# Kernel optimization log

Hardware: AMD Instinct MI355X
Metric: run time of the kernel (lower is better)

## Reference

```python
import jax, jax.numpy as jnp
import numpy as np

B, L, P, W, T = 2048, 128, 8, 512, 128
DT = 0.01


def setup_inputs() -> dict:
    key = jax.random.key(0)
    ks = jax.random.split(key, 8)
    def lin(k, fan_in, fan_out):
        return jax.random.normal(k, (fan_out, fan_in), jnp.float32) / jnp.sqrt(jnp.float32(fan_in))
    return {
        "x0": jax.random.normal(ks[0], (B, L), jnp.float32),
        "ts": jnp.arange(T, dtype=jnp.float32) * DT,
        "args": jax.random.normal(ks[1], (B, P), jnp.float32),
        "W0": lin(ks[2], L + P, W), "b0": jnp.zeros((W,), jnp.float32),
        "W1": lin(ks[3], W, W),     "b1": jnp.zeros((W,), jnp.float32),
        "W2": lin(ks[4], W, L),     "b2": jnp.zeros((L,), jnp.float32),
    }


def _vf(y, args, W0, b0, W1, b1, W2, b2):
    # OdeMLP: concat state with params, then Linear/tanh MLP. y:[B,L], args:[B,P]
    h = jnp.concatenate([y, args], axis=-1)
    h = jnp.tanh(h @ W0.T + b0)
    h = jnp.tanh(h @ W1.T + b1)
    return h @ W2.T + b2


def reference(x0, ts, args, W0, b0, W1, b1, W2, b2):
    # Fixed-step Bosh3 (Bogacki-Shampine 3rd order) integration, saving at every ts.
    f = lambda y: _vf(y, args, W0, b0, W1, b1, W2, b2)
    dts = ts[1:] - ts[:-1]  # [T-1]

    def step(y, dt):
        k1 = f(y)
        k2 = f(y + 0.5 * dt * k1)
        k3 = f(y + 0.75 * dt * k2)
        y_next = y + dt * ((2.0 / 9.0) * k1 + (1.0 / 3.0) * k2 + (4.0 / 9.0) * k3)
        return y_next, y_next

    _, ys = jax.lax.scan(step, x0, dts)          # [T-1, B, L]
    ys = jnp.concatenate([x0[None], ys], axis=0)  # [T, B, L]
    return jnp.transpose(ys, (1, 0, 2))           # [B, T, L]
```

## Files before the change

kernel.cpp:

```cpp
#include <hip/hip_runtime.h>
#include <hip/hip_bf16.h>


#define B_ 2048
#define L_ 128
#define P_ 8
#define T_ 128
#define GT_ 64
#define NGRP (B_/GT_)
#define NBLK (NGRP*8)

typedef __attribute__((ext_vector_type(8))) short short8;
typedef __attribute__((ext_vector_type(4))) float f32x4;
typedef __attribute__((ext_vector_type(4))) unsigned int u32x4;

#define WTOT (800*512)
#define CNT_OFF (WTOT + 256)
#define EXB (CNT_OFF + 16384)
#define XSTR 160
#define GSTR (64*XSTR + 2*64*512)

#define VMW0 asm volatile("s_waitcnt vmcnt(0)" ::: "memory")
#define LKW0 asm volatile("s_waitcnt lgkmcnt(0)" ::: "memory")
#define SCHB __builtin_amdgcn_sched_barrier(0)

__device__ __forceinline__ unsigned short f2bf(float f){
  unsigned u = __builtin_bit_cast(unsigned, f);
  u += 0x7fffu + ((u >> 16) & 1u);
  return (unsigned short)(u >> 16);
}

__device__ __forceinline__ float tanh_fast(float x){
  float e = __expf(2.0f * x);
  return 1.0f - __fdividef(2.0f, e + 1.0f);
}

__device__ __forceinline__ short8 ld_dev(const unsigned short* p){
  u32x4 r;
  asm volatile("global_load_dwordx4 %0, %1, off sc0 sc1"
               : "=v"(r) : "v"(p) : "memory");
  return __builtin_bit_cast(short8, r);
}
__device__ __forceinline__ void st_dev16b(unsigned short* p, u32x4 v){
  asm volatile("global_store_dwordx4 %0, %1, off sc0 sc1"
               :: "v"(p), "v"(v) : "memory");
}
__device__ __forceinline__ void st_dev2(unsigned short* p, unsigned short v){
  unsigned vv = v;
  asm volatile("global_store_short %0, %1, off sc0 sc1"
               :: "v"(p), "v"(vv) : "memory");
}

__global__ void prep_weights(const float* __restrict__ W0,
                             const float* __restrict__ W1,
                             const float* __restrict__ W2,
                             const float* __restrict__ ts,
                             unsigned short* __restrict__ wp){
  int idx = blockIdx.x * blockDim.x + threadIdx.x;
  if (idx >= WTOT){
    int t = idx - WTOT;
    if (t < T_ - 1){
      float* dts = (float*)(wp + WTOT);
      dts[t] = ts[t+1] - ts[t];
    } else if (t >= T_ && t < T_ + 8192){
      ((unsigned*)(wp + CNT_OFF))[t - T_] = 0u;
    }
    return;
  }
  int e = idx & 511, f = idx >> 9;
  int j = e & 7, lane = e >> 3;
  int m = f / 100, r = f % 100;
  const float* src; int nt, kt, Korig;
  if (r < 20)      { src = W0; Korig = 136; nt = 4*m + r/5;        kt = r%5; }
  else if (r < 84) { int q = r-20; src = W1; Korig = 512; nt = 4*m + (q>>4); kt = q&15; }
  else             { src = W2; Korig = 512; nt = m;                kt = r-84; }
  int row = nt*16 + (lane & 15);
  int k   = kt*32 + ((lane >> 4) << 3) + j;
  float v = (k < Korig) ? src[row*Korig + k] : 0.0f;
  wp[idx] = f2bf(v);
}

__global__ __launch_bounds__(256, 1)
void ode_main(const float* __restrict__ x0,
              const float* __restrict__ args,
              const float* __restrict__ b0, const float* __restrict__ b1,
              const float* __restrict__ b2,
              unsigned short* wp,
              float* __restrict__ out){
  __shared__ __align__(16) unsigned short wlds[100*512];
  __shared__ __align__(16) unsigned short hstg[4][16][64];
  __shared__ float dtl[T_];

  const int tid  = threadIdx.x;
  const int lane = tid & 63;
  const int wv   = tid >> 6;
  const int lo   = lane & 15;
  const int hi   = lane >> 4;
  const int bid  = blockIdx.x;
  const int m    = (bid >> 3) & 7;
  const int g    = (bid & 7)*4 + (bid >> 6);
  const int r0   = g * GT_;

  unsigned* cnt = (unsigned*)(wp + CNT_OFF) + (g*4 + wv)*64;
  unsigned short* gx  = wp + EXB + (size_t)g * GSTR;
  unsigned short* h1b = gx  + 64*XSTR;
  unsigned short* h2b = h1b + 64*512;

  {
    const u32x4* s = (const u32x4*)(wp + (size_t)m * 51200);
    u32x4* d = (u32x4*)wlds;
    for (int i = tid; i < 6400; i += 256) d[i] = s[i];
  }
  if (tid < T_-1) dtl[tid] = ((const float*)(wp + WTOT))[tid];

  float b0v[4], b1v[4];
  #pragma unroll
  for (int n = 0; n < 4; ++n){
    b0v[n] = b0[(4*m + n)*16 + lo];
    b1v[n] = b1[(4*m + n)*16 + lo];
  }
  const int c3 = m*16 + lo;
  float b2v = b2[c3];

  float yr[4], yn[4];
  #pragma unroll
  for (int j = 0; j < 4; ++j){
    int row = wv*16 + 4*hi + j;
    float v = x0[(r0 + row)*L_ + c3];
    yr[j] = v;
    __builtin_nontemporal_store(v, &out[((r0 + row)*T_ + 0)*L_ + c3]);
    st_dev2(gx + row*XSTR + c3, f2bf(v));
  }
  if (m == 0){
    #pragma unroll
    for (int e = 0; e < 8; ++e){
      int idx = lane*8 + e;
      int row = wv*16 + (idx >> 5), cc = 128 + (idx & 31);
      unsigned short vv = (cc < 136) ? f2bf(args[(r0 + row)*P_ + (cc - 128)])
                                     : (unsigned short)0;
      st_dev2(gx + row*XSTR + cc, vv);
    }
  }
  __syncthreads();

  unsigned tgt = 8;
  auto sigpoll = [&]{
    if (lane == 0)
      __hip_atomic_fetch_add(cnt, 1u, __ATOMIC_RELAXED, __HIP_MEMORY_SCOPE_AGENT);
    unsigned v;
    do {
      v = 0;
      if (lane == 0)
        v = __hip_atomic_load(cnt, __ATOMIC_RELAXED, __HIP_MEMORY_SCOPE_AGENT);
      v = __shfl(v, 0);
      if (v < tgt) __builtin_amdgcn_s_sleep(1);
    } while (v < tgt);
    tgt += 8;
  };

  VMW0;
  sigpoll();

  const int arow = wv*16 + lo;
  const int aoff = hi << 3;
  const int r16 = lane >> 2, ch4 = lane & 3;
  const int xr16 = (lane & 31) >> 1, xch = lane & 1;

  auto publish_h = [&](unsigned short* hb){
    LKW0;
    u32x4 v0 = *(const u32x4*)&hstg[wv][r16][ch4*16];
    u32x4 v1 = *(const u32x4*)&hstg[wv][r16][ch4*16 + 8];
    unsigned short* dst = hb + (wv*16 + r16)*512 + m*64 + ch4*16;
    st_dev16b(dst, v0);
    st_dev16b(dst + 8, v1);
    VMW0;
  };

  auto phase1 = [&]{
    short8 xa[5];
    #pragma unroll
    for (int kt = 0; kt < 5; ++kt)
      xa[kt] = ld_dev(gx + arow*XSTR + kt*32 + aoff);
    VMW0; SCHB;
    f32x4 acc[4];
    #pragma unroll
    for (int n = 0; n < 4; ++n) acc[n] = f32x4{0,0,0,0};
    #pragma unroll
    for (int kt = 0; kt < 5; ++kt)
      #pragma unroll
      for (int n = 0; n < 4; ++n){
        short8 wf = *(const short8*)(wlds + (n*5 + kt)*512 + lane*8);
        acc[n] = __builtin_amdgcn_mfma_f32_16x16x32_bf16(xa[kt], wf, acc[n], 0, 0, 0);
      }
    #pragma unroll
    for (int n = 0; n < 4; ++n)
      #pragma unroll
      for (int j = 0; j < 4; ++j)
        hstg[wv][4*hi + j][n*16 + lo] = f2bf(tanh_fast(acc[n][j] + b0v[n]));
    publish_h(h1b);
    sigpoll();
  };

  auto phase2 = [&]{
    short8 ha[16];
    #pragma unroll
    for (int kt = 0; kt < 16; ++kt)
      ha[kt] = ld_dev(h1b + arow*512 + kt*32 + aoff);
    VMW0; SCHB;
    f32x4 acc[4];
    #pragma unroll
    for (int n = 0; n < 4; ++n) acc[n] = f32x4{0,0,0,0};
    #pragma unroll
    for (int kt = 0; kt < 16; ++kt)
      #pragma unroll
      for (int n = 0; n < 4; ++n){
        short8 wf = *(const short8*)(wlds + (20 + n*16 + kt)*512 + lane*8);
        acc[n] = __builtin_amdgcn_mfma_f32_16x16x32_bf16(ha[kt], wf, acc[n], 0, 0, 0);
      }
    #pragma unroll
    for (int n = 0; n < 4; ++n)
      #pragma unroll
      for (int j = 0; j < 4; ++j)
        hstg[wv][4*hi + j][n*16 + lo] = f2bf(tanh_fast(acc[n][j] + b1v[n]));
    publish_h(h2b);
    sigpoll();
  };

  for (int t = 1; t < T_; ++t){
    float dt = dtl[t-1];
    #pragma unroll 1
    for (int s = 0; s < 3; ++s){
      phase1();
      phase2();
      short8 h2a[16];
      #pragma unroll
      for (int kt = 0; kt < 16; ++kt)
        h2a[kt] = ld_dev(h2b + arow*512 + kt*32 + aoff);
      VMW0; SCHB;
      f32x4 a3 = f32x4{0,0,0,0};
      #pragma unroll
      for (int kt = 0; kt < 16; ++kt){
        short8 wf = *(const short8*)(wlds + (84 + kt)*512 + lane*8);
        a3 = __builtin_amdgcn_mfma_f32_16x16x32_bf16(h2a[kt], wf, a3, 0, 0, 0);
      }
      #pragma unroll
      for (int j = 0; j < 4; ++j){
        float k = a3[j] + b2v;
        float xs;
        if (s == 0){ yn[j] = yr[j] + dt*(2.0f/9.0f)*k; xs = yr[j] + 0.5f*dt*k; }
        else if (s == 1){ yn[j] += dt*(1.0f/3.0f)*k;   xs = yr[j] + 0.75f*dt*k; }
        else { yn[j] += dt*(4.0f/9.0f)*k; yr[j] = yn[j]; xs = yr[j]; }
        hstg[wv][4*hi + j][lo] = f2bf(xs);
      }
      LKW0;
      if (lane < 32){
        u32x4 v = *(const u32x4*)&hstg[wv][xr16][xch*8];
        st_dev16b(gx + (wv*16 + xr16)*XSTR + m*16 + xch*8, v);
      }
      VMW0;
      if (lane == 0)
        __hip_atomic_fetch_add(cnt, 1u, __ATOMIC_RELAXED, __HIP_MEMORY_SCOPE_AGENT);
      if (s == 2){
        #pragma unroll
        for (int j = 0; j < 4; ++j){
          int row = wv*16 + 4*hi + j;
          __builtin_nontemporal_store(yr[j], &out[((r0 + row)*T_ + t)*L_ + c3]);
        }
      }
      {
        unsigned v;
        do {
          v = 0;
          if (lane == 0)
            v = __hip_atomic_load(cnt, __ATOMIC_RELAXED, __HIP_MEMORY_SCOPE_AGENT);
          v = __shfl(v, 0);
          if (v < tgt) __builtin_amdgcn_s_sleep(1);
        } while (v < tgt);
        tgt += 8;
      }
    }
  }
}

extern "C" void kernel_launch(void* const* d_in, const int* in_sizes, int n_in,
                              void* d_out, int out_size, void* d_ws, size_t ws_size,
                              hipStream_t stream) {
  const float* x0   = (const float*)d_in[0];
  const float* ts   = (const float*)d_in[1];
  const float* args = (const float*)d_in[2];
  const float* W0   = (const float*)d_in[3];
  const float* b0   = (const float*)d_in[4];
  const float* W1   = (const float*)d_in[5];
  const float* b1   = (const float*)d_in[6];
  const float* W2   = (const float*)d_in[7];
  const float* b2   = (const float*)d_in[8];
  unsigned short* wp = (unsigned short*)d_ws;
  float* out = (float*)d_out;

  prep_weights<<<(WTOT + T_ + 8192 + 255)/256, 256, 0, stream>>>(W0, W1, W2, ts, wp);
  ode_main<<<NBLK, 256, 0, stream>>>(x0, args, b0, b1, b2, wp, out);
}
```

Before: 4.643 ms.

## Detect same-XCC groups at runtime and use L2-scoped coherent exchange loads/stores

Blocks are remapped so that m = bid>>5 and g = bid&31, which is meant to place all 8 blocks of a batch group on the same XCC. At startup each group checks this: every block reads its XCC id, the m==0 block writes a tag, and the others compare against it. If all 8 blocks agree, the exchange traffic uses sc0-only loads and stores, keeping it in the shared L2 instead of going through system-coherent sc1 accesses. Otherwise the kernel falls back to the old path. This relies on the dispatcher placing blocks round-robin across XCCs, and it adds a handshake at startup.

```diff
diff --git a/kernel.cpp b/kernel.cpp
--- a/kernel.cpp
+++ b/kernel.cpp
@@ -1,5 +1,6 @@
 #include <hip/hip_runtime.h>
 #include <hip/hip_bf16.h>
+#include <type_traits>
 
 
 #define B_ 2048
@@ -8,7 +9,7 @@
 #define T_ 128
 #define GT_ 64
 #define NGRP (B_/GT_)
-#define NBLK (NGRP*8)
+#define NBLK 256
 
 typedef __attribute__((ext_vector_type(8))) short short8;
 typedef __attribute__((ext_vector_type(4))) float f32x4;
@@ -16,9 +17,10 @@
 
 #define WTOT (800*512)
 #define CNT_OFF (WTOT + 256)
-#define EXB (CNT_OFF + 16384)
+#define EXB (CNT_OFF + 16768)
 #define XSTR 160
 #define GSTR (64*XSTR + 2*64*512)
+#define NZERO 8320
 
 #define VMW0 asm volatile("s_waitcnt vmcnt(0)" ::: "memory")
 #define LKW0 asm volatile("s_waitcnt lgkmcnt(0)" ::: "memory")
@@ -35,20 +37,23 @@
   return 1.0f - __fdividef(2.0f, e + 1.0f);
 }
 
-__device__ __forceinline__ short8 ld_dev(const unsigned short* p){
+template<bool COH> __device__ __forceinline__ short8 ld_ex(const unsigned short* p){
   u32x4 r;
-  asm volatile("global_load_dwordx4 %0, %1, off sc0 sc1"
-               : "=v"(r) : "v"(p) : "memory");
+  if constexpr (COH)
+    asm volatile("global_load_dwordx4 %0, %1, off sc0" : "=v"(r) : "v"(p) : "memory");
+  else
+    asm volatile("global_load_dwordx4 %0, %1, off sc0 sc1" : "=v"(r) : "v"(p) : "memory");
   return __builtin_bit_cast(short8, r);
 }
-__device__ __forceinline__ void st_dev16b(unsigned short* p, u32x4 v){
-  asm volatile("global_store_dwordx4 %0, %1, off sc0 sc1"
-               :: "v"(p), "v"(v) : "memory");
-}
-__device__ __forceinline__ void st_dev2(unsigned short* p, unsigned short v){
+template<bool COH> __device__ __forceinline__ void st_ex16(unsigned short* p, u32x4 v){
+  if constexpr (COH)
+    asm volatile("global_store_dwordx4 %0, %1, off sc0" :: "v"(p), "v"(v) : "memory");
+  else
+    asm volatile("global_store_dwordx4 %0, %1, off sc0 sc1" :: "v"(p), "v"(v) : "memory");
+}
+__device__ __forceinline__ void st2_l3(unsigned short* p, unsigned short v){
   unsigned vv = v;
-  asm volatile("global_store_short %0, %1, off sc0 sc1"
-               :: "v"(p), "v"(vv) : "memory");
+  asm volatile("global_store_short %0, %1, off sc0 sc1" :: "v"(p), "v"(vv) : "memory");
 }
 
 __global__ void prep_weights(const float* __restrict__ W0,
@@ -62,7 +67,7 @@
     if (t < T_ - 1){
       float* dts = (float*)(wp + WTOT);
       dts[t] = ts[t+1] - ts[t];
-    } else if (t >= T_ && t < T_ + 8192){
+    } else if (t >= T_ && t < T_ + NZERO){
       ((unsigned*)(wp + CNT_OFF))[t - T_] = 0u;
     }
     return;
@@ -90,6 +95,7 @@
   __shared__ __align__(16) unsigned short wlds[100*512];
   __shared__ __align__(16) unsigned short hstg[4][16][64];
   __shared__ float dtl[T_];
+  __shared__ unsigned cohsh;
 
   const int tid  = threadIdx.x;
   const int lane = tid & 63;
@@ -97,11 +103,13 @@
   const int lo   = lane & 15;
   const int hi   = lane >> 4;
   const int bid  = blockIdx.x;
-  const int m    = (bid >> 3) & 7;
-  const int g    = (bid & 7)*4 + (bid >> 6);
+  const int m    = bid >> 5;
+  const int g    = bid & 31;
   const int r0   = g * GT_;
 
   unsigned* cnt = (unsigned*)(wp + CNT_OFF) + (g*4 + wv)*64;
+  unsigned* tsl = (unsigned*)(wp + CNT_OFF) + 8192 + g;
+  unsigned* vc  = (unsigned*)(wp + CNT_OFF) + 8256 + g;
   unsigned short* gx  = wp + EXB + (size_t)g * GSTR;
   unsigned short* h1b = gx  + 64*XSTR;
   unsigned short* h2b = h1b + 64*512;
@@ -121,6 +129,10 @@
   }
   const int c3 = m*16 + lo;
   float b2v = b2[c3];
+
+  unsigned xcc;
+  asm volatile("s_getreg_b32 %0, hwreg(HW_REG_XCC_ID)" : "=s"(xcc));
+  xcc &= 0xFu;
 
   float yr[4], yn[4];
   #pragma unroll
@@ -129,7 +141,7 @@
     float v = x0[(r0 + row)*L_ + c3];
     yr[j] = v;
     __builtin_nontemporal_store(v, &out[((r0 + row)*T_ + 0)*L_ + c3]);
-    st_dev2(gx + row*XSTR + c3, f2bf(v));
+    st2_l3(gx + row*XSTR + c3, f2bf(v));
   }
   if (m == 0){
     #pragma unroll
@@ -138,148 +150,192 @@
       int row = wv*16 + (idx >> 5), cc = 128 + (idx & 31);
       unsigned short vv = (cc < 136) ? f2bf(args[(r0 + row)*P_ + (cc - 128)])
                                      : (unsigned short)0;
-      st_dev2(gx + row*XSTR + cc, vv);
+      st2_l3(gx + row*XSTR + cc, vv);
     }
   }
   __syncthreads();
 
-  unsigned tgt = 8;
-  auto sigpoll = [&]{
-    if (lane == 0)
-      __hip_atomic_fetch_add(cnt, 1u, __ATOMIC_RELAXED, __HIP_MEMORY_SCOPE_AGENT);
+  VMW0;
+  if (lane == 0)
+    __hip_atomic_fetch_add(cnt, 1u, __ATOMIC_RELAXED, __HIP_MEMORY_SCOPE_AGENT);
+  {
     unsigned v;
     do {
       v = 0;
       if (lane == 0)
         v = __hip_atomic_load(cnt, __ATOMIC_RELAXED, __HIP_MEMORY_SCOPE_AGENT);
       v = __shfl(v, 0);
-      if (v < tgt) __builtin_amdgcn_s_sleep(1);
-    } while (v < tgt);
-    tgt += 8;
-  };
-
-  VMW0;
-  sigpoll();
+      if (v < 8) __builtin_amdgcn_s_sleep(1);
+    } while (v < 8);
+  }
+
+  if (wv == 0){
+    if (m == 0 && lane == 0){
+      unsigned mg = 0xC0DE0000u | xcc;
+      asm volatile("global_store_dword %0, %1, off sc0" :: "v"(tsl), "v"(mg) : "memory");
+    }
+    VMW0;
+    unsigned v = 0;
+    if (lane == 0){
+      for (int it = 0; it < (1<<16); ++it){
+        unsigned tv;
+        asm volatile("global_load_dword %0, %1, off sc0" : "=v"(tv) : "v"(tsl) : "memory");
+        VMW0;
+        if (tv == (0xC0DE0000u | xcc)){ v = 1; break; }
+        __builtin_amdgcn_s_sleep(2);
+      }
+      __hip_atomic_fetch_add(vc, 1u + (v << 8), __ATOMIC_RELAXED, __HIP_MEMORY_SCOPE_AGENT);
+      unsigned c;
+      do {
+        c = __hip_atomic_load(vc, __ATOMIC_RELAXED, __HIP_MEMORY_SCOPE_AGENT);
+        if ((c & 0xFFu) < 8) __builtin_amdgcn_s_sleep(2);
+      } while ((c & 0xFFu) < 8);
+      cohsh = ((c >> 8) == 8u);
+    }
+  }
+  __syncthreads();
+  const unsigned coh = cohsh;
 
   const int arow = wv*16 + lo;
   const int aoff = hi << 3;
   const int r16 = lane >> 2, ch4 = lane & 3;
   const int xr16 = (lane & 31) >> 1, xch = lane & 1;
 
-  auto publish_h = [&](unsigned short* hb){
-    LKW0;
-    u32x4 v0 = *(const u32x4*)&hstg[wv][r16][ch4*16];
-    u32x4 v1 = *(const u32x4*)&hstg[wv][r16][ch4*16 + 8];
-    unsigned short* dst = hb + (wv*16 + r16)*512 + m*64 + ch4*16;
-    st_dev16b(dst, v0);
-    st_dev16b(dst + 8, v1);
-    VMW0;
-  };
-
-  auto phase1 = [&]{
-    short8 xa[5];
-    #pragma unroll
-    for (int kt = 0; kt < 5; ++kt)
-      xa[kt] = ld_dev(gx + arow*XSTR + kt*32 + aoff);
-    VMW0; SCHB;
-    f32x4 acc[4];
-    #pragma unroll
-    for (int n = 0; n < 4; ++n) acc[n] = f32x4{0,0,0,0};
-    #pragma unroll
-    for (int kt = 0; kt < 5; ++kt)
-      #pragma unroll
-      for (int n = 0; n < 4; ++n){
-        short8 wf = *(const short8*)(wlds + (n*5 + kt)*512 + lane*8);
-        acc[n] = __builtin_amdgcn_mfma_f32_16x16x32_bf16(xa[kt], wf, acc[n], 0, 0, 0);
-      }
-    #pragma unroll
-    for (int n = 0; n < 4; ++n)
-      #pragma unroll
-      for (int j = 0; j < 4; ++j)
-        hstg[wv][4*hi + j][n*16 + lo] = f2bf(tanh_fast(acc[n][j] + b0v[n]));
-    publish_h(h1b);
-    sigpoll();
-  };
-
-  auto phase2 = [&]{
-    short8 ha[16];
-    #pragma unroll
-    for (int kt = 0; kt < 16; ++kt)
-      ha[kt] = ld_dev(h1b + arow*512 + kt*32 + aoff);
-    VMW0; SCHB;
-    f32x4 acc[4];
-    #pragma unroll
-    for (int n = 0; n < 4; ++n) acc[n] = f32x4{0,0,0,0};
-    #pragma unroll
-    for (int kt = 0; kt < 16; ++kt)
-      #pragma unroll
-      for (int n = 0; n < 4; ++n){
-        short8 wf = *(const short8*)(wlds + (20 + n*16 + kt)*512 + lane*8);
-        acc[n] = __builtin_amdgcn_mfma_f32_16x16x32_bf16(ha[kt], wf, acc[n], 0, 0, 0);
-      }
-    #pragma unroll
-    for (int n = 0; n < 4; ++n)
-      #pragma unroll
-      for (int j = 0; j < 4; ++j)
-        hstg[wv][4*hi + j][n*16 + lo] = f2bf(tanh_fast(acc[n][j] + b1v[n]));
-    publish_h(h2b);
-    sigpoll();
-  };
-
-  for (int t = 1; t < T_; ++t){
-    float dt = dtl[t-1];
-    #pragma unroll 1
-    for (int s = 0; s < 3; ++s){
-      phase1();
-      phase2();
-      short8 h2a[16];
-      #pragma unroll
-      for (int kt = 0; kt < 16; ++kt)
-        h2a[kt] = ld_dev(h2b + arow*512 + kt*32 + aoff);
-      VMW0; SCHB;
-      f32x4 a3 = f32x4{0,0,0,0};
-      #pragma unroll
-      for (int kt = 0; kt < 16; ++kt){
-        short8 wf = *(const short8*)(wlds + (84 + kt)*512 + lane*8);
-        a3 = __builtin_amdgcn_mfma_f32_16x16x32_bf16(h2a[kt], wf, a3, 0, 0, 0);
-      }
-      #pragma unroll
-      for (int j = 0; j < 4; ++j){
-        float k = a3[j] + b2v;
-        float xs;
-        if (s == 0){ yn[j] = yr[j] + dt*(2.0f/9.0f)*k; xs = yr[j] + 0.5f*dt*k; }
-        else if (s == 1){ yn[j] += dt*(1.0f/3.0f)*k;   xs = yr[j] + 0.75f*dt*k; }
-        else { yn[j] += dt*(4.0f/9.0f)*k; yr[j] = yn[j]; xs = yr[j]; }
-        hstg[wv][4*hi + j][lo] = f2bf(xs);
-      }
-      LKW0;
-      if (lane < 32){
-        u32x4 v = *(const u32x4*)&hstg[wv][xr16][xch*8];
-        st_dev16b(gx + (wv*16 + xr16)*XSTR + m*16 + xch*8, v);
-      }
-      VMW0;
+  auto run = [&](auto coh_t){
+    constexpr bool COH = decltype(coh_t)::value;
+    unsigned tgt = 16;
+    auto sigpoll = [&]{
       if (lane == 0)
         __hip_atomic_fetch_add(cnt, 1u, __ATOMIC_RELAXED, __HIP_MEMORY_SCOPE_AGENT);
-      if (s == 2){
+      unsigned v;
+      do {
+        v = 0;
+        if (lane == 0)
+          v = __hip_atomic_load(cnt, __ATOMIC_RELAXED, __HIP_MEMORY_SCOPE_AGENT);
+        v = __shfl(v, 0);
+        if (v < tgt) __builtin_amdgcn_s_sleep(1);
+      } while (v < tgt);
+      tgt += 8;
+    };
+
+    auto publish_h = [&](unsigned short* hb){
+      LKW0;
+      u32x4 v0 = *(const u32x4*)&hstg[wv][r16][ch4*16];
+      u32x4 v1 = *(const u32x4*)&hstg[wv][r16][ch4*16 + 8];
+      unsigned short* dst = hb + (wv*16 + r16)*512 + m*64 + ch4*16;
+      st_ex16<COH>(dst, v0);
+      st_ex16<COH>(dst + 8, v1);
+      VMW0;
+    };
+
+    auto phase1 = [&]{
+      short8 xa[5];
+      #pragma unroll
+      for (int kt = 0; kt < 5; ++kt)
+        xa[kt] = ld_ex<COH>(gx + arow*XSTR + kt*32 + aoff);
+      VMW0; SCHB;
+      f32x4 acc[4];
+      #pragma unroll
+      for (int n = 0; n < 4; ++n) acc[n] = f32x4{0,0,0,0};
+      #pragma unroll
+      for (int kt = 0; kt < 5; ++kt)
+        #pragma unroll
+        for (int n = 0; n < 4; ++n){
+          short8 wf = *(const short8*)(wlds + (n*5 + kt)*512 + lane*8);
+          acc[n] = __builtin_amdgcn_mfma_f32_16x16x32_bf16(xa[kt], wf, acc[n], 0, 0, 0);
+        }
+      #pragma unroll
+      for (int n = 0; n < 4; ++n)
+        #pragma unroll
+        for (int j = 0; j < 4; ++j)
+          hstg[wv][4*hi + j][n*16 + lo] = f2bf(tanh_fast(acc[n][j] + b0v[n]));
+      publish_h(h1b);
+      sigpoll();
+    };
+
+    auto phase2 = [&]{
+      short8 ha[16];
+      #pragma unroll
+      for (int kt = 0; kt < 16; ++kt)
+        ha[kt] = ld_ex<COH>(h1b + arow*512 + kt*32 + aoff);
+      VMW0; SCHB;
+      f32x4 acc[4];
+      #pragma unroll
+      for (int n = 0; n < 4; ++n) acc[n] = f32x4{0,0,0,0};
+      #pragma unroll
+      for (int kt = 0; kt < 16; ++kt)
+        #pragma unroll
+        for (int n = 0; n < 4; ++n){
+          short8 wf = *(const short8*)(wlds + (20 + n*16 + kt)*512 + lane*8);
+          acc[n] = __builtin_amdgcn_mfma_f32_16x16x32_bf16(ha[kt], wf, acc[n], 0, 0, 0);
+        }
+      #pragma unroll
+      for (int n = 0; n < 4; ++n)
+        #pragma unroll
+        for (int j = 0; j < 4; ++j)
+          hstg[wv][4*hi + j][n*16 + lo] = f2bf(tanh_fast(acc[n][j] + b1v[n]));
+      publish_h(h2b);
+      sigpoll();
+    };
+
+    for (int t = 1; t < T_; ++t){
+      float dt = dtl[t-1];
+      #pragma unroll 1
+      for (int s = 0; s < 3; ++s){
+        phase1();
+        phase2();
+        short8 h2a[16];
+        #pragma unroll
+        for (int kt = 0; kt < 16; ++kt)
+          h2a[kt] = ld_ex<COH>(h2b + arow*512 + kt*32 + aoff);
+        VMW0; SCHB;
+        f32x4 a3 = f32x4{0,0,0,0};
+        #pragma unroll
+        for (int kt = 0; kt < 16; ++kt){
+          short8 wf = *(const short8*)(wlds + (84 + kt)*512 + lane*8);
+          a3 = __builtin_amdgcn_mfma_f32_16x16x32_bf16(h2a[kt], wf, a3, 0, 0, 0);
+        }
         #pragma unroll
         for (int j = 0; j < 4; ++j){
-          int row = wv*16 + 4*hi + j;
-          __builtin_nontemporal_store(yr[j], &out[((r0 + row)*T_ + t)*L_ + c3]);
+          float k = a3[j] + b2v;
+          float xs;
+          if (s == 0){ yn[j] = yr[j] + dt*(2.0f/9.0f)*k; xs = yr[j] + 0.5f*dt*k; }
+          else if (s == 1){ yn[j] += dt*(1.0f/3.0f)*k;   xs = yr[j] + 0.75f*dt*k; }
+          else { yn[j] += dt*(4.0f/9.0f)*k; yr[j] = yn[j]; xs = yr[j]; }
+          hstg[wv][4*hi + j][lo] = f2bf(xs);
+        }
+        LKW0;
+        if (lane < 32){
+          u32x4 v = *(const u32x4*)&hstg[wv][xr16][xch*8];
+          st_ex16<COH>(gx + (wv*16 + xr16)*XSTR + m*16 + xch*8, v);
+        }
+        VMW0;
+        if (lane == 0)
+          __hip_atomic_fetch_add(cnt, 1u, __ATOMIC_RELAXED, __HIP_MEMORY_SCOPE_AGENT);
+        if (s == 2){
+          #pragma unroll
+          for (int j = 0; j < 4; ++j){
+            int row = wv*16 + 4*hi + j;
+            __builtin_nontemporal_store(yr[j], &out[((r0 + row)*T_ + t)*L_ + c3]);
+          }
+        }
+        {
+          unsigned v;
+          do {
+            v = 0;
+            if (lane == 0)
+              v = __hip_atomic_load(cnt, __ATOMIC_RELAXED, __HIP_MEMORY_SCOPE_AGENT);
+            v = __shfl(v, 0);
+            if (v < tgt) __builtin_amdgcn_s_sleep(1);
+          } while (v < tgt);
+          tgt += 8;
         }
       }
-      {
-        unsigned v;
-        do {
-          v = 0;
-          if (lane == 0)
-            v = __hip_atomic_load(cnt, __ATOMIC_RELAXED, __HIP_MEMORY_SCOPE_AGENT);
-          v = __shfl(v, 0);
-          if (v < tgt) __builtin_amdgcn_s_sleep(1);
-        } while (v < tgt);
-        tgt += 8;
-      }
-    }
-  }
+    }
+  };
+
+  if (coh) run(std::integral_constant<bool, true>{});
+  else     run(std::integral_constant<bool, false>{});
 }
 
 extern "C" void kernel_launch(void* const* d_in, const int* in_sizes, int n_in,
@@ -297,6 +353,6 @@
   unsigned short* wp = (unsigned short*)d_ws;
   float* out = (float*)d_out;
 
-  prep_weights<<<(WTOT + T_ + 8192 + 255)/256, 256, 0, stream>>>(W0, W1, W2, ts, wp);
+  prep_weights<<<(WTOT + T_ + NZERO + 255)/256, 256, 0, stream>>>(W0, W1, W2, ts, wp);
   ode_main<<<NBLK, 256, 0, stream>>>(x0, args, b0, b1, b2, wp, out);
 }
```

Result: slower. 13.87 ms (+198.7%).
